# Performance work log

Measured on AMD Instinct MI355X. Metric: run time of the kernel, lower is better.

Reference implementation:

```python
import jax, jax.numpy as jnp
import numpy as np

N = 65536
EMB_DIM = 1024
PICK_NUM = 12  # ceil(ln(65536)) = ceil(11.09) = 12


def setup_inputs() -> dict:
    key = jax.random.key(0)
    k_emb, k_wq, k_bq, k_wk, k_bk, k_idx = jax.random.split(key, 6)
    s = 1.0 / np.sqrt(EMB_DIM)
    embed_matrix = jax.random.normal(k_emb, (N, EMB_DIM), dtype=jnp.float32)
    Wq = jax.random.normal(k_wq, (EMB_DIM, EMB_DIM), dtype=jnp.float32) * s
    bq = jax.random.normal(k_bq, (EMB_DIM,), dtype=jnp.float32) * s
    Wk = jax.random.normal(k_wk, (EMB_DIM, EMB_DIM), dtype=jnp.float32) * s
    bk = jax.random.normal(k_bk, (EMB_DIM,), dtype=jnp.float32) * s
    # np.random.choice(n, pick_num, replace=False) -> deterministic permutation slice
    indices = jax.random.permutation(k_idx, N)[:PICK_NUM].astype(jnp.int32)
    return {"embed_matrix": embed_matrix, "Wq": Wq, "bq": bq,
            "Wk": Wk, "bk": bk, "indices": indices}


def reference(embed_matrix, Wq, bq, Wk, bk, indices):
    pick_num = indices.shape[0]
    # torch.nn.Linear: y = x @ W.T + b
    query = embed_matrix @ Wq.T + bq          # [n, d]
    key = embed_matrix @ Wk.T + bk            # [n, d]
    new_key = key[indices]                    # [pick, d] sampled keys
    Q_K_sample = query @ new_key.T            # [n, pick]
    max_values = jnp.max(Q_K_sample, axis=1)  # [n]
    _, top_indices = jax.lax.top_k(max_values, pick_num)
    Q_reduced = query[top_indices]            # [pick, d]
    Q_K = Q_reduced @ key.T                   # [pick, n]
    pooled = jnp.max(Q_K, axis=0, keepdims=True)  # [1, n]
    attention_embed = pooled @ embed_matrix   # [1, d]
    return attention_embed
```

## Files before the change

### kernel.cpp

```cpp
#include <hip/hip_runtime.h>

#define DIM 1024
#define NROWS 65536
#define PICK 12


__global__ void __launch_bounds__(256)
rows12_kernel(const float* __restrict__ emb, const float* __restrict__ W,
              const float* __restrict__ b, const int* __restrict__ idx,
              float* __restrict__ out) {
    int d = blockIdx.x;
    int t = threadIdx.x;
    int lane = t & 63;
    int q = t >> 6;
    int e0 = q * 256 + lane * 4;
    float4 w4 = *(const float4*)&W[(size_t)d * DIM + e0];
    float part[PICK];
#pragma unroll
    for (int j = 0; j < PICK; ++j) {
        int r = idx[j];
        float4 e4 = *(const float4*)&emb[(size_t)r * DIM + e0];
        part[j] = w4.x * e4.x + w4.y * e4.y + w4.z * e4.z + w4.w * e4.w;
    }
#pragma unroll
    for (int j = 0; j < PICK; ++j) {
        float v = part[j];
        for (int s = 32; s > 0; s >>= 1) v += __shfl_down(v, s, 64);
        part[j] = v;
    }
    __shared__ float red[4][PICK];
    if (lane == 0) {
#pragma unroll
        for (int j = 0; j < PICK; ++j) red[q][j] = part[j];
    }
    __syncthreads();
    if (t < PICK) {
        float s = red[0][t] + red[1][t] + red[2][t] + red[3][t] + b[d];
        out[t * DIM + d] = s;
    }
}

__global__ void __launch_bounds__(256)
colmat_kernel(const float* __restrict__ W, const float* __restrict__ V,
              const float* __restrict__ b, float* __restrict__ out,
              float* __restrict__ cvec) {
    int blk = blockIdx.x;
    int t = threadIdx.x;
    if (blk == 32) {
        float part[PICK];
#pragma unroll
        for (int j = 0; j < PICK; ++j) part[j] = 0.f;
        for (int k = 0; k < 4; ++k) {
            int d = t + k * 256;
            float bv = b[d];
#pragma unroll
            for (int j = 0; j < PICK; ++j) part[j] += bv * V[j * DIM + d];
        }
#pragma unroll
        for (int j = 0; j < PICK; ++j) {
            float v = part[j];
            for (int s = 32; s > 0; s >>= 1) v += __shfl_down(v, s, 64);
            if ((t & 63) == 0) atomicAdd(&cvec[j], v);
        }
        return;
    }
    int eg = blk & 3;
    int dg = blk >> 2;
    int e = eg * 256 + t;
    int d0 = dg * 128;
    __shared__ float Vs[PICK][128];
    for (int i = t; i < PICK * 128; i += 256) {
        int j = i >> 7, dd = i & 127;
        Vs[j][dd] = V[j * DIM + d0 + dd];
    }
    __syncthreads();
    float acc[PICK];
#pragma unroll
    for (int j = 0; j < PICK; ++j) acc[j] = 0.f;
    for (int dd = 0; dd < 128; ++dd) {
        float w = W[(size_t)(d0 + dd) * DIM + e];
#pragma unroll
        for (int j = 0; j < PICK; ++j) acc[j] += w * Vs[j][dd];
    }
#pragma unroll
    for (int j = 0; j < PICK; ++j) atomicAdd(&out[e * PICK + j], acc[j]);
}

__global__ void __launch_bounds__(256)
pass1_kernel(const float* __restrict__ emb, const float* __restrict__ M,
             const float* __restrict__ c0, float* __restrict__ maxv) {
    int t = threadIdx.x;
    int lane = t & 63;
    int q = __builtin_amdgcn_readfirstlane(t >> 6);
    int row = blockIdx.x * 64 + lane;
    const float* erow = emb + (size_t)row * DIM + q * 256;
    const float* Mq = M + (size_t)q * 256 * PICK;
    float acc[PICK];
#pragma unroll
    for (int j = 0; j < PICK; ++j) acc[j] = 0.f;
    for (int e = 0; e < 256; e += 4) {
        float4 v = *(const float4*)(erow + e);
        const float* m = Mq + e * PICK;
#pragma unroll
        for (int j = 0; j < PICK; ++j)
            acc[j] += v.x * m[j] + v.y * m[j + 12] + v.z * m[j + 24] + v.w * m[j + 36];
    }
    __shared__ float red[4][64][PICK + 1];
#pragma unroll
    for (int j = 0; j < PICK; ++j) red[q][lane][j] = acc[j];
    __syncthreads();
    if (t < 64) {
        float mx = -3e38f;
#pragma unroll
        for (int j = 0; j < PICK; ++j) {
            float s = red[0][t][j] + red[1][t][j] + red[2][t][j] + red[3][t][j] + c0[j];
            mx = fmaxf(mx, s);
        }
        maxv[blockIdx.x * 64 + t] = mx;
    }
}

__global__ void __launch_bounds__(256)
pass2_kernel(const float* __restrict__ emb, const float* __restrict__ Rt,
             const float* __restrict__ c1, float* __restrict__ out) {
    int t = threadIdx.x;
    int lane = t & 63;
    int q = __builtin_amdgcn_readfirstlane(t >> 6);
    int row = blockIdx.x * 64 + lane;
    const float* erow = emb + (size_t)row * DIM + q * 256;
    const float* Mq = Rt + (size_t)q * 256 * PICK;
    float acc[PICK];
#pragma unroll
    for (int j = 0; j < PICK; ++j) acc[j] = 0.f;
    for (int e = 0; e < 256; e += 4) {
        float4 v = *(const float4*)(erow + e);
        const float* m = Mq + e * PICK;
#pragma unroll
        for (int j = 0; j < PICK; ++j)
            acc[j] += v.x * m[j] + v.y * m[j + 12] + v.z * m[j + 24] + v.w * m[j + 36];
    }
    __shared__ float red[4][64][PICK + 1];
    __shared__ float pool[64];
#pragma unroll
    for (int j = 0; j < PICK; ++j) red[q][lane][j] = acc[j];
    __syncthreads();
    if (t < 64) {
        float mx = -3e38f;
#pragma unroll
        for (int j = 0; j < PICK; ++j) {
            float s = red[0][t][j] + red[1][t][j] + red[2][t][j] + red[3][t][j] + c1[j];
            mx = fmaxf(mx, s);
        }
        pool[t] = mx;
    }
    __syncthreads();
    const float* ep = emb + (size_t)blockIdx.x * 64 * DIM + t * 4;
    float ax = 0.f, ay = 0.f, az = 0.f, aw = 0.f;
    for (int r = 0; r < 64; ++r) {
        float p = pool[r];
        float4 v = *(const float4*)(ep + (size_t)r * DIM);
        ax += p * v.x; ay += p * v.y; az += p * v.z; aw += p * v.w;
    }
    atomicAdd(&out[t * 4 + 0], ax);
    atomicAdd(&out[t * 4 + 1], ay);
    atomicAdd(&out[t * 4 + 2], az);
    atomicAdd(&out[t * 4 + 3], aw);
}

__global__ void __launch_bounds__(256)
top12_local(const float* __restrict__ maxv, float* __restrict__ cand_v,
            int* __restrict__ cand_i) {
    int t = threadIdx.x;
    int base = blockIdx.x * 256;
    __shared__ float mv[256];
    __shared__ float sv[256];
    __shared__ int si[256];
    mv[t] = maxv[base + t];
    __syncthreads();
    for (int k = 0; k < PICK; ++k) {
        sv[t] = mv[t]; si[t] = t;
        __syncthreads();
        for (int s = 128; s > 0; s >>= 1) {
            if (t < s) {
                if (sv[t + s] > sv[t] || (sv[t + s] == sv[t] && si[t + s] < si[t])) {
                    sv[t] = sv[t + s]; si[t] = si[t + s];
                }
            }
            __syncthreads();
        }
        if (t == 0) {
            cand_v[blockIdx.x * PICK + k] = sv[0];
            cand_i[blockIdx.x * PICK + k] = base + si[0];
            mv[si[0]] = -3e38f;
        }
        __syncthreads();
    }
}

__global__ void __launch_bounds__(256)
top12_merge(const float* __restrict__ cand_v, const int* __restrict__ cand_i,
            int* __restrict__ top_idx) {
    int t = threadIdx.x;
    __shared__ float mv[3072];
    __shared__ int mi[3072];
    __shared__ float sv[256];
    __shared__ int si[256];
    __shared__ int sl[256];
    for (int i = t; i < 3072; i += 256) { mv[i] = cand_v[i]; mi[i] = cand_i[i]; }
    __syncthreads();
    for (int k = 0; k < PICK; ++k) {
        float bv = -3e38f; int bi = 0x7fffffff; int bl = -1;
        for (int i = t; i < 3072; i += 256) {
            float v = mv[i]; int ii = mi[i];
            if (v > bv || (v == bv && ii < bi)) { bv = v; bi = ii; bl = i; }
        }
        sv[t] = bv; si[t] = bi; sl[t] = bl;
        __syncthreads();
        for (int s = 128; s > 0; s >>= 1) {
            if (t < s) {
                if (sv[t + s] > sv[t] || (sv[t + s] == sv[t] && si[t + s] < si[t])) {
                    sv[t] = sv[t + s]; si[t] = si[t + s]; sl[t] = sl[t + s];
                }
            }
            __syncthreads();
        }
        if (t == 0) { top_idx[k] = si[0]; mv[sl[0]] = -3e38f; }
        __syncthreads();
    }
}

extern "C" void kernel_launch(void* const* d_in, const int* in_sizes, int n_in,
                              void* d_out, int out_size, void* d_ws, size_t ws_size,
                              hipStream_t stream) {
    const float* emb = (const float*)d_in[0];
    const float* Wq  = (const float*)d_in[1];
    const float* bq  = (const float*)d_in[2];
    const float* Wk  = (const float*)d_in[3];
    const float* bk  = (const float*)d_in[4];
    const int* indices = (const int*)d_in[5];
    float* out = (float*)d_out;
    float* ws = (float*)d_ws;

    float* NK      = ws;
    float* Qr      = ws + 12288;
    float* M       = ws + 24576;
    float* Rt      = ws + 36864;
    float* c0      = ws + 49152;
    float* c1      = ws + 49168;
    float* cand_v  = ws + 49184;
    int*   cand_i  = (int*)(ws + 52256);
    int*   top_idx = (int*)(ws + 55328);
    float* maxv    = ws + 55344;

    hipMemsetAsync(M, 0, (size_t)(12288 * 2 + 32) * sizeof(float), stream);
    hipMemsetAsync(out, 0, DIM * sizeof(float), stream);

    rows12_kernel<<<1024, 256, 0, stream>>>(emb, Wk, bk, indices, NK);
    colmat_kernel<<<33, 256, 0, stream>>>(Wq, NK, bq, M, c0);
    pass1_kernel<<<1024, 256, 0, stream>>>(emb, M, c0, maxv);
    top12_local<<<256, 256, 0, stream>>>(maxv, cand_v, cand_i);
    top12_merge<<<1, 256, 0, stream>>>(cand_v, cand_i, top_idx);
    rows12_kernel<<<1024, 256, 0, stream>>>(emb, Wq, bq, top_idx, Qr);
    colmat_kernel<<<33, 256, 0, stream>>>(Wk, Qr, bk, Rt, c1);
    pass2_kernel<<<1024, 256, 0, stream>>>(emb, Rt, c1, out);
}
```

Before: 681.9 us.

## Keep projection matrix in registers and stream rows with wave-level reductions

Pass1 and pass2 are restructured so each 64-lane wave holds a 16x6 slice of the projection matrix in registers and streams the block's 64 embedding rows coalesced, with register double-buffered prefetch and shuffle-xor reductions across the wave. This replaces the per-thread strided row reads and repeated matrix reloads. Pass2 fuses the pooled weighted row sum into the same streaming loop, with a per-row block barrier. Colmat now launches 129 blocks over smaller row chunks for more parallelism, and the top-k local stage uses 64 larger blocks so the merge has fewer candidates. Costs are high register pressure, many shuffles per row, and a barrier per row in pass2.

After: 723.4 us. 6.1% more time.

```diff
diff --git a/kernel.cpp b/kernel.cpp
--- a/kernel.cpp
+++ b/kernel.cpp
@@ -46,7 +46,7 @@
               float* __restrict__ cvec) {
     int blk = blockIdx.x;
     int t = threadIdx.x;
-    if (blk == 32) {
+    if (blk == 128) {
         float part[PICK];
 #pragma unroll
         for (int j = 0; j < PICK; ++j) part[j] = 0.f;
@@ -67,17 +67,17 @@
     int eg = blk & 3;
     int dg = blk >> 2;
     int e = eg * 256 + t;
-    int d0 = dg * 128;
-    __shared__ float Vs[PICK][128];
-    for (int i = t; i < PICK * 128; i += 256) {
-        int j = i >> 7, dd = i & 127;
+    int d0 = dg * 32;
+    __shared__ float Vs[PICK][32];
+    for (int i = t; i < PICK * 32; i += 256) {
+        int j = i >> 5, dd = i & 31;
         Vs[j][dd] = V[j * DIM + d0 + dd];
     }
     __syncthreads();
     float acc[PICK];
 #pragma unroll
     for (int j = 0; j < PICK; ++j) acc[j] = 0.f;
-    for (int dd = 0; dd < 128; ++dd) {
+    for (int dd = 0; dd < 32; ++dd) {
         float w = W[(size_t)(d0 + dd) * DIM + e];
 #pragma unroll
         for (int j = 0; j < PICK; ++j) acc[j] += w * Vs[j][dd];
@@ -86,99 +86,148 @@
     for (int j = 0; j < PICK; ++j) atomicAdd(&out[e * PICK + j], acc[j]);
 }
 
-__global__ void __launch_bounds__(256)
+__global__ void __launch_bounds__(128)
 pass1_kernel(const float* __restrict__ emb, const float* __restrict__ M,
              const float* __restrict__ c0, float* __restrict__ maxv) {
     int t = threadIdx.x;
     int lane = t & 63;
-    int q = __builtin_amdgcn_readfirstlane(t >> 6);
-    int row = blockIdx.x * 64 + lane;
-    const float* erow = emb + (size_t)row * DIM + q * 256;
-    const float* Mq = M + (size_t)q * 256 * PICK;
-    float acc[PICK];
-#pragma unroll
-    for (int j = 0; j < PICK; ++j) acc[j] = 0.f;
-    for (int e = 0; e < 256; e += 4) {
-        float4 v = *(const float4*)(erow + e);
-        const float* m = Mq + e * PICK;
-#pragma unroll
-        for (int j = 0; j < PICK; ++j)
-            acc[j] += v.x * m[j] + v.y * m[j + 12] + v.z * m[j + 24] + v.w * m[j + 36];
-    }
-    __shared__ float red[4][64][PICK + 1];
-#pragma unroll
-    for (int j = 0; j < PICK; ++j) red[q][lane][j] = acc[j];
-    __syncthreads();
-    if (t < 64) {
-        float mx = -3e38f;
-#pragma unroll
-        for (int j = 0; j < PICK; ++j) {
-            float s = red[0][t][j] + red[1][t][j] + red[2][t][j] + red[3][t][j] + c0[j];
-            mx = fmaxf(mx, s);
-        }
-        maxv[blockIdx.x * 64 + t] = mx;
-    }
-}
-
-__global__ void __launch_bounds__(256)
+    int h = t >> 6;
+    float m[16][6];
+#pragma unroll
+    for (int c = 0; c < 4; ++c)
+#pragma unroll
+        for (int x = 0; x < 4; ++x) {
+            const float* mp = M + (size_t)(c * 256 + lane * 4 + x) * PICK + h * 6;
+#pragma unroll
+            for (int jj = 0; jj < 6; ++jj) m[c * 4 + x][jj] = mp[jj];
+        }
+    float cb[6];
+#pragma unroll
+    for (int jj = 0; jj < 6; ++jj) cb[jj] = c0[h * 6 + jj];
+    __shared__ float mbuf[2][64];
+    const float* base = emb + (size_t)blockIdx.x * 64 * DIM + lane * 4;
+    float4 cur[4];
+#pragma unroll
+    for (int c = 0; c < 4; ++c) cur[c] = *(const float4*)(base + c * 256);
+    for (int r = 0; r < 64; ++r) {
+        float4 nxt[4];
+        const float* nb = base + (size_t)(r + 1 < 64 ? r + 1 : r) * DIM;
+#pragma unroll
+        for (int c = 0; c < 4; ++c) nxt[c] = *(const float4*)(nb + c * 256);
+        float acc[6];
+#pragma unroll
+        for (int jj = 0; jj < 6; ++jj)
+            acc[jj] = cur[0].x * m[0][jj] + cur[0].y * m[1][jj] +
+                      cur[0].z * m[2][jj] + cur[0].w * m[3][jj] +
+                      cur[1].x * m[4][jj] + cur[1].y * m[5][jj] +
+                      cur[1].z * m[6][jj] + cur[1].w * m[7][jj] +
+                      cur[2].x * m[8][jj] + cur[2].y * m[9][jj] +
+                      cur[2].z * m[10][jj] + cur[2].w * m[11][jj] +
+                      cur[3].x * m[12][jj] + cur[3].y * m[13][jj] +
+                      cur[3].z * m[14][jj] + cur[3].w * m[15][jj];
+#pragma unroll
+        for (int s = 1; s < 64; s <<= 1)
+#pragma unroll
+            for (int jj = 0; jj < 6; ++jj) acc[jj] += __shfl_xor(acc[jj], s, 64);
+        float mx = acc[0] + cb[0];
+#pragma unroll
+        for (int jj = 1; jj < 6; ++jj) mx = fmaxf(mx, acc[jj] + cb[jj]);
+        if (lane == 0) mbuf[h][r] = mx;
+#pragma unroll
+        for (int c = 0; c < 4; ++c) cur[c] = nxt[c];
+    }
+    __syncthreads();
+    if (t < 64) maxv[blockIdx.x * 64 + t] = fmaxf(mbuf[0][t], mbuf[1][t]);
+}
+
+__global__ void __launch_bounds__(128)
 pass2_kernel(const float* __restrict__ emb, const float* __restrict__ Rt,
              const float* __restrict__ c1, float* __restrict__ out) {
     int t = threadIdx.x;
     int lane = t & 63;
-    int q = __builtin_amdgcn_readfirstlane(t >> 6);
-    int row = blockIdx.x * 64 + lane;
-    const float* erow = emb + (size_t)row * DIM + q * 256;
-    const float* Mq = Rt + (size_t)q * 256 * PICK;
-    float acc[PICK];
-#pragma unroll
-    for (int j = 0; j < PICK; ++j) acc[j] = 0.f;
-    for (int e = 0; e < 256; e += 4) {
-        float4 v = *(const float4*)(erow + e);
-        const float* m = Mq + e * PICK;
-#pragma unroll
-        for (int j = 0; j < PICK; ++j)
-            acc[j] += v.x * m[j] + v.y * m[j + 12] + v.z * m[j + 24] + v.w * m[j + 36];
-    }
-    __shared__ float red[4][64][PICK + 1];
-    __shared__ float pool[64];
-#pragma unroll
-    for (int j = 0; j < PICK; ++j) red[q][lane][j] = acc[j];
-    __syncthreads();
-    if (t < 64) {
-        float mx = -3e38f;
-#pragma unroll
-        for (int j = 0; j < PICK; ++j) {
-            float s = red[0][t][j] + red[1][t][j] + red[2][t][j] + red[3][t][j] + c1[j];
-            mx = fmaxf(mx, s);
-        }
-        pool[t] = mx;
-    }
-    __syncthreads();
-    const float* ep = emb + (size_t)blockIdx.x * 64 * DIM + t * 4;
-    float ax = 0.f, ay = 0.f, az = 0.f, aw = 0.f;
+    int h = t >> 6;
+    float m[16][6];
+#pragma unroll
+    for (int c = 0; c < 4; ++c)
+#pragma unroll
+        for (int x = 0; x < 4; ++x) {
+            const float* mp = Rt + (size_t)(c * 256 + lane * 4 + x) * PICK + h * 6;
+#pragma unroll
+            for (int jj = 0; jj < 6; ++jj) m[c * 4 + x][jj] = mp[jj];
+        }
+    float cb[6];
+#pragma unroll
+    for (int jj = 0; jj < 6; ++jj) cb[jj] = c1[h * 6 + jj];
+    __shared__ float xbuf[2][2];
+    const float* base = emb + (size_t)blockIdx.x * 64 * DIM + lane * 4;
+    float4 cur[4];
+#pragma unroll
+    for (int c = 0; c < 4; ++c) cur[c] = *(const float4*)(base + c * 256);
+    float o[2][4];
+#pragma unroll
+    for (int ci = 0; ci < 2; ++ci)
+#pragma unroll
+        for (int x = 0; x < 4; ++x) o[ci][x] = 0.f;
     for (int r = 0; r < 64; ++r) {
-        float p = pool[r];
-        float4 v = *(const float4*)(ep + (size_t)r * DIM);
-        ax += p * v.x; ay += p * v.y; az += p * v.z; aw += p * v.w;
-    }
-    atomicAdd(&out[t * 4 + 0], ax);
-    atomicAdd(&out[t * 4 + 1], ay);
-    atomicAdd(&out[t * 4 + 2], az);
-    atomicAdd(&out[t * 4 + 3], aw);
+        float4 nxt[4];
+        const float* nb = base + (size_t)(r + 1 < 64 ? r + 1 : r) * DIM;
+#pragma unroll
+        for (int c = 0; c < 4; ++c) nxt[c] = *(const float4*)(nb + c * 256);
+        float acc[6];
+#pragma unroll
+        for (int jj = 0; jj < 6; ++jj)
+            acc[jj] = cur[0].x * m[0][jj] + cur[0].y * m[1][jj] +
+                      cur[0].z * m[2][jj] + cur[0].w * m[3][jj] +
+                      cur[1].x * m[4][jj] + cur[1].y * m[5][jj] +
+                      cur[1].z * m[6][jj] + cur[1].w * m[7][jj] +
+                      cur[2].x * m[8][jj] + cur[2].y * m[9][jj] +
+                      cur[2].z * m[10][jj] + cur[2].w * m[11][jj] +
+                      cur[3].x * m[12][jj] + cur[3].y * m[13][jj] +
+                      cur[3].z * m[14][jj] + cur[3].w * m[15][jj];
+#pragma unroll
+        for (int s = 1; s < 64; s <<= 1)
+#pragma unroll
+            for (int jj = 0; jj < 6; ++jj) acc[jj] += __shfl_xor(acc[jj], s, 64);
+        float mxh = acc[0] + cb[0];
+#pragma unroll
+        for (int jj = 1; jj < 6; ++jj) mxh = fmaxf(mxh, acc[jj] + cb[jj]);
+        int p = r & 1;
+        if (lane == 0) xbuf[p][h] = mxh;
+        __syncthreads();
+        float mx = fmaxf(xbuf[p][0], xbuf[p][1]);
+#pragma unroll
+        for (int ci = 0; ci < 2; ++ci) {
+            float4 v = cur[2 * h + ci];
+            o[ci][0] += mx * v.x; o[ci][1] += mx * v.y;
+            o[ci][2] += mx * v.z; o[ci][3] += mx * v.w;
+        }
+#pragma unroll
+        for (int c = 0; c < 4; ++c) cur[c] = nxt[c];
+    }
+#pragma unroll
+    for (int ci = 0; ci < 2; ++ci)
+#pragma unroll
+        for (int x = 0; x < 4; ++x)
+            atomicAdd(&out[(2 * h + ci) * 256 + lane * 4 + x], o[ci][x]);
 }
 
 __global__ void __launch_bounds__(256)
 top12_local(const float* __restrict__ maxv, float* __restrict__ cand_v,
             int* __restrict__ cand_i) {
     int t = threadIdx.x;
-    int base = blockIdx.x * 256;
-    __shared__ float mv[256];
+    int base = blockIdx.x * 1024;
+    __shared__ float mv[1024];
     __shared__ float sv[256];
     __shared__ int si[256];
-    mv[t] = maxv[base + t];
+    for (int i = t; i < 1024; i += 256) mv[i] = maxv[base + i];
     __syncthreads();
     for (int k = 0; k < PICK; ++k) {
-        sv[t] = mv[t]; si[t] = t;
+        float bv = -3e38f; int bi = 0x7fffffff;
+        for (int i = t; i < 1024; i += 256) {
+            float v = mv[i];
+            if (v > bv || (v == bv && base + i < bi)) { bv = v; bi = base + i; }
+        }
+        sv[t] = bv; si[t] = bi;
         __syncthreads();
         for (int s = 128; s > 0; s >>= 1) {
             if (t < s) {
@@ -190,8 +239,8 @@
         }
         if (t == 0) {
             cand_v[blockIdx.x * PICK + k] = sv[0];
-            cand_i[blockIdx.x * PICK + k] = base + si[0];
-            mv[si[0]] = -3e38f;
+            cand_i[blockIdx.x * PICK + k] = si[0];
+            mv[si[0] - base] = -3e38f;
         }
         __syncthreads();
     }
@@ -201,16 +250,16 @@
 top12_merge(const float* __restrict__ cand_v, const int* __restrict__ cand_i,
             int* __restrict__ top_idx) {
     int t = threadIdx.x;
-    __shared__ float mv[3072];
-    __shared__ int mi[3072];
+    __shared__ float mv[768];
+    __shared__ int mi[768];
     __shared__ float sv[256];
     __shared__ int si[256];
     __shared__ int sl[256];
-    for (int i = t; i < 3072; i += 256) { mv[i] = cand_v[i]; mi[i] = cand_i[i]; }
+    for (int i = t; i < 768; i += 256) { mv[i] = cand_v[i]; mi[i] = cand_i[i]; }
     __syncthreads();
     for (int k = 0; k < PICK; ++k) {
         float bv = -3e38f; int bi = 0x7fffffff; int bl = -1;
-        for (int i = t; i < 3072; i += 256) {
+        for (int i = t; i < 768; i += 256) {
             float v = mv[i]; int ii = mi[i];
             if (v > bv || (v == bv && ii < bi)) { bv = v; bi = ii; bl = i; }
         }
@@ -248,19 +297,19 @@
     float* c0      = ws + 49152;
     float* c1      = ws + 49168;
     float* cand_v  = ws + 49184;
-    int*   cand_i  = (int*)(ws + 52256);
-    int*   top_idx = (int*)(ws + 55328);
-    float* maxv    = ws + 55344;
+    int*   cand_i  = (int*)(ws + 49952);
+    int*   top_idx = (int*)(ws + 50720);
+    float* maxv    = ws + 50736;
 
     hipMemsetAsync(M, 0, (size_t)(12288 * 2 + 32) * sizeof(float), stream);
     hipMemsetAsync(out, 0, DIM * sizeof(float), stream);
 
     rows12_kernel<<<1024, 256, 0, stream>>>(emb, Wk, bk, indices, NK);
-    colmat_kernel<<<33, 256, 0, stream>>>(Wq, NK, bq, M, c0);
-    pass1_kernel<<<1024, 256, 0, stream>>>(emb, M, c0, maxv);
-    top12_local<<<256, 256, 0, stream>>>(maxv, cand_v, cand_i);
+    colmat_kernel<<<129, 256, 0, stream>>>(Wq, NK, bq, M, c0);
+    pass1_kernel<<<1024, 128, 0, stream>>>(emb, M, c0, maxv);
+    top12_local<<<64, 256, 0, stream>>>(maxv, cand_v, cand_i);
     top12_merge<<<1, 256, 0, stream>>>(cand_v, cand_i, top_idx);
     rows12_kernel<<<1024, 256, 0, stream>>>(emb, Wq, bq, top_idx, Qr);
-    colmat_kernel<<<33, 256, 0, stream>>>(Wk, Qr, bk, Rt, c1);
-    pass2_kernel<<<1024, 256, 0, stream>>>(emb, Rt, c1, out);
-}
+    colmat_kernel<<<129, 256, 0, stream>>>(Wk, Qr, bk, Rt, c1);
+    pass2_kernel<<<1024, 128, 0, stream>>>(emb, Rt, c1, out);
+}
```
